# Performance work log

Hardware: AMD Instinct MI355X
Metric: run time of the kernel (lower is better)

Reference implementation:

```python
import jax, jax.numpy as jnp
import numpy as np

MASK_PROPORTION = 0.5
NEG_BIG = -99999999.0


def setup_inputs() -> dict:
    key = jax.random.key(0)
    k_x, k_w1, k_b1, k_w2, k_b2 = jax.random.split(key, 5)
    B, T, D, H = 32, 4096, 1024, 256
    x = jax.random.normal(k_x, (B, T, D), dtype=jnp.float32)
    s1 = 1.0 / np.sqrt(D)
    s2 = 1.0 / np.sqrt(H)
    W1 = jax.random.uniform(k_w1, (D, H), minval=-s1, maxval=s1, dtype=jnp.float32)
    b1 = jax.random.uniform(k_b1, (H,), minval=-s1, maxval=s1, dtype=jnp.float32)
    W2 = jax.random.uniform(k_w2, (H, 1), minval=-s2, maxval=s2, dtype=jnp.float32)
    b2 = jax.random.uniform(k_b2, (1,), minval=-s2, maxval=s2, dtype=jnp.float32)
    return {"x": x, "W1": W1, "b1": b1, "W2": W2, "b2": b2}


def reference(x, W1, b1, W2, b2):
    # e: [B, T, 1] attention scores from small MLP
    h = jnp.tanh(jnp.einsum("btd,dh->bth", x, W1) + b1)
    e = jnp.einsum("bth,ho->bto", h, W2) + b2  # [B, T, 1]

    T = e.shape[1]
    threshold_index = int(T * MASK_PROPORTION)
    sorted_e = jnp.sort(e, axis=1)
    threshold_value = sorted_e[:, threshold_index]          # [B, 1]
    # mask: +1 where e < threshold (kept), NEG_BIG where e >= threshold
    mask = jnp.where(e >= threshold_value[:, None, :], NEG_BIG, 1.0)
    e = e + mask
    beta = jax.nn.softmax(e, axis=1)                        # [B, T, 1]
    # bmm(beta^T, x) -> [B, 1, D], permute -> [B, D, 1], unsqueeze -> [B, D, 1, 1]
    out = jnp.einsum("bto,btd->bd", beta, x)
    return out[:, :, None, None]
```

## Files before the change

### kernel.cpp

```cpp
#include <hip/hip_runtime.h>
#include <hip/hip_bf16.h>
#include <math.h>

#define B_   32
#define T_   4096
#define D_   1024
#define H_   256
#define KTH  2048
#define SC   64
#define BM   128
#define BKE  32
#define NTE  (D_/BKE)
#define ABUF (BM*BKE)
#define BBUF (H_*BKE)
#define EPSB 4.0e-3f
#define MAXBAND 256
#define RB   4

typedef __attribute__((ext_vector_type(8))) short short8;
typedef __attribute__((ext_vector_type(4))) float f32x4;

#define FENCE4() asm volatile("s_waitcnt vmcnt(4) lgkmcnt(0)" ::: "memory")
#define FENCE0() asm volatile("s_waitcnt vmcnt(0) lgkmcnt(0)" ::: "memory")
#define BARRIER() __builtin_amdgcn_s_barrier()
#define SCHED()  __builtin_amdgcn_sched_barrier(0)
#define GLL(src, dst) __builtin_amdgcn_global_load_lds( \
    (const __attribute__((address_space(1))) unsigned int*)(src), \
    (__attribute__((address_space(3))) unsigned int*)(dst), 16, 0, 0)

__device__ inline unsigned f2s(float f) {
    unsigned u = __float_as_uint(f);
    return (u & 0x80000000u) ? ~u : (u | 0x80000000u);
}
__device__ inline float s2f(unsigned s) {
    unsigned x = (s & 0x80000000u) ? (s & 0x7fffffffu) : ~s;
    return __uint_as_float(x);
}
__device__ inline unsigned f2bf_rne(float f) {
    unsigned u = __float_as_uint(f);
    return (u + 0x7FFFu + ((u >> 16) & 1u)) >> 16;
}
__device__ inline unsigned pk2(float a, float b) {
    return f2bf_rne(a) | (f2bf_rne(b) << 16);
}
__device__ inline int block_sum_i(int v, int* sb, int tid) {
    #pragma unroll
    for (int o = 32; o; o >>= 1) v += __shfl_down(v, o);
    __syncthreads();
    if ((tid & 63) == 0) sb[tid >> 6] = v;
    __syncthreads();
    return sb[0] + sb[1] + sb[2] + sb[3];
}
__device__ inline float block_max_f(float v, float* sb, int tid) {
    #pragma unroll
    for (int o = 32; o; o >>= 1) v = fmaxf(v, __shfl_down(v, o));
    __syncthreads();
    if ((tid & 63) == 0) sb[tid >> 6] = v;
    __syncthreads();
    return fmaxf(fmaxf(sb[0], sb[1]), fmaxf(sb[2], sb[3]));
}
__device__ inline float block_sum_f(float v, float* sb, int tid) {
    #pragma unroll
    for (int o = 32; o; o >>= 1) v += __shfl_down(v, o);
    __syncthreads();
    if ((tid & 63) == 0) sb[tid >> 6] = v;
    __syncthreads();
    return sb[0] + sb[1] + sb[2] + sb[3];
}

__global__ __launch_bounds__(256) void k_w1t(const float* __restrict__ W1,
                                             ushort* __restrict__ Whi) {
    __shared__ float tile[32][33];
    const int kb = blockIdx.x * 32, nb = blockIdx.y * 32;
    const int tx = threadIdx.x & 31, ty = threadIdx.x >> 5;
    #pragma unroll
    for (int i = 0; i < 4; i++)
        tile[ty + 8*i][tx] = W1[(long)(kb + ty + 8*i) * H_ + nb + tx];
    __syncthreads();
    #pragma unroll
    for (int i = 0; i < 4; i++) {
        long o = (long)(nb + ty + 8*i) * D_ + kb + tx;
        Whi[o] = (ushort)f2bf_rne(tile[tx][ty + 8*i]);
    }
}

__global__ __launch_bounds__(512, 4) void k_e_mfma(
    const float* __restrict__ x,
    const ushort* __restrict__ Whi,
    const float* __restrict__ b1, const float* __restrict__ W2,
    const float* __restrict__ b2, float* __restrict__ e_out)
{
    __shared__ ushort sA[2][ABUF];
    __shared__ ushort sB[3][BBUF];
    __shared__ float  sRed[4][BM];

    const int tid  = threadIdx.x;
    const int lane = tid & 63;
    const int wv   = tid >> 6;
    const int wm   = wv >> 2, wn = wv & 3;
    const int l15  = lane & 15, lg = lane >> 4;
    const long row0 = (long)blockIdx.x * BM;

    const int ar = tid >> 2, aj = tid & 3;
    const float* aga = x + (row0 + ar) * (long)D_ + aj * 8;
    const int awo = (ar >> 4) * 512 + aj * 128 + (ar & 15) * 8;

    const int c0 = tid, c1 = tid + 512;
    const int bn0 = (c0 >> 6) * 16 + (c0 & 15), bk0 = (c0 >> 4) & 3;
    const int bn1 = (c1 >> 6) * 16 + (c1 & 15), bk1 = (c1 >> 4) & 3;
    const ushort* bga0 = Whi + (long)bn0 * D_ + bk0 * 8;
    const ushort* bga1 = Whi + (long)bn1 * D_ + bk1 * 8;
    const int bdst0 = c0 * 8, bdst1 = c1 * 8;

    int aoff[4], boff[4];
    #pragma unroll
    for (int fm = 0; fm < 4; fm++)
        aoff[fm] = (wm * 4 + fm) * 512 + lg * 128 + l15 * 8;
    #pragma unroll
    for (int fn = 0; fn < 4; fn++)
        boff[fn] = (wn * 4 + fn) * 512 + lg * 128 + l15 * 8;

    f32x4 acc[4][4];
    #pragma unroll
    for (int i = 0; i < 4; i++)
        #pragma unroll
        for (int j = 0; j < 4; j++) acc[i][j] = (f32x4){0.f, 0.f, 0.f, 0.f};

    ushort* sBb = (ushort*)sB;
    auto stageB = [&](int ko, int bi) {
        GLL(bga0 + ko, sBb + bi * BBUF + bdst0);
        GLL(bga1 + ko, sBb + bi * BBUF + bdst1);
    };
    auto writeA = [&](ushort* dst, const float4& a0, const float4& a1) {
        uint4 ap = make_uint4(pk2(a0.x, a0.y), pk2(a0.z, a0.w),
                              pk2(a1.x, a1.y), pk2(a1.z, a1.w));
        *(uint4*)&dst[awo] = ap;
    };
    auto compute = [&](const ushort* sa, const ushort* sb) {
        short8 bfr[4];
        #pragma unroll
        for (int fn = 0; fn < 4; fn++)
            bfr[fn] = *(const short8*)&sb[boff[fn]];
        __builtin_amdgcn_s_setprio(1);
        #pragma unroll
        for (int fm = 0; fm < 4; fm++) {
            short8 afr = *(const short8*)&sa[aoff[fm]];
            #pragma unroll
            for (int fn = 0; fn < 4; fn++)
                acc[fm][fn] = __builtin_amdgcn_mfma_f32_16x16x32_bf16(afr, bfr[fn], acc[fm][fn], 0, 0, 0);
        }
        __builtin_amdgcn_s_setprio(0);
    };

    float4 rA0a = *(const float4*)(aga);
    float4 rA0b = *(const float4*)(aga + 4);
    stageB(0, 0);
    float4 rA1a = *(const float4*)(aga + BKE);
    float4 rA1b = *(const float4*)(aga + BKE + 4);
    stageB(BKE, 1);
    writeA(sA[0], rA0a, rA0b);

    #pragma unroll 3
    for (int t = 0; t < NTE - 2; t += 2) {
        FENCE4(); BARRIER(); SCHED();
        {
            const int ko = (t + 2) * BKE;
            rA0a = *(const float4*)(aga + ko);
            rA0b = *(const float4*)(aga + ko + 4);
            stageB(ko, (t + 2) % 3);
            compute(sA[0], sBb + (t % 3) * BBUF);
            writeA(sA[1], rA1a, rA1b);
        }
        FENCE4(); BARRIER(); SCHED();
        {
            const int ko = (t + 3) * BKE;
            rA1a = *(const float4*)(aga + ko);
            rA1b = *(const float4*)(aga + ko + 4);
            stageB(ko, (t + 3) % 3);
            compute(sA[1], sBb + ((t + 1) % 3) * BBUF);
            writeA(sA[0], rA0a, rA0b);
        }
    }
    FENCE4(); BARRIER(); SCHED();
    compute(sA[0], sBb + ((NTE - 2) % 3) * BBUF);
    writeA(sA[1], rA1a, rA1b);
    FENCE0(); BARRIER(); SCHED();
    compute(sA[1], sBb + ((NTE - 1) % 3) * BBUF);

    float b1v[4], w2v[4];
    #pragma unroll
    for (int fn = 0; fn < 4; fn++) {
        int j = wn * 64 + fn * 16 + l15;
        b1v[fn] = b1[j]; w2v[fn] = W2[j];
    }
    #pragma unroll
    for (int fm = 0; fm < 4; fm++) {
        #pragma unroll
        for (int r = 0; r < 4; r++) {
            float s = 0.f;
            #pragma unroll
            for (int fn = 0; fn < 4; fn++)
                s += tanhf(acc[fm][fn][r] + b1v[fn]) * w2v[fn];
            s += __shfl_xor(s, 1); s += __shfl_xor(s, 2);
            s += __shfl_xor(s, 4); s += __shfl_xor(s, 8);
            if (l15 == 0) sRed[wn][wm * 64 + fm * 16 + lg * 4 + r] = s;
        }
    }
    __syncthreads();
    if (tid < BM)
        e_out[row0 + tid] = sRed[0][tid] + sRed[1][tid] + sRed[2][tid] + sRed[3][tid] + b2[0];
}

template<int BUILD>
__global__ __launch_bounds__(256) void k_thresh(const float* __restrict__ e,
                                                int* __restrict__ counts,
                                                int* __restrict__ list,
                                                int* __restrict__ sidx,
                                                float* __restrict__ sval,
                                                int* __restrict__ scount) {
    __shared__ int   sbi[4];
    __shared__ float sbf[4];
    __shared__ int   wsum[4];
    __shared__ int   scnt;
    const int b = blockIdx.x, tid = threadIdx.x;
    const int lane = tid & 63, wid = tid >> 6;
    const float* eb = e + (long)b * T_;
    const int t0 = tid * 16;

    float fe[16]; unsigned ue[16];
    #pragma unroll
    for (int i = 0; i < 16; i += 4) {
        float4 v = *(const float4*)(eb + t0 + i);
        fe[i] = v.x; fe[i+1] = v.y; fe[i+2] = v.z; fe[i+3] = v.w;
    }
    #pragma unroll
    for (int i = 0; i < 16; i++) ue[i] = f2s(fe[i]);

    unsigned lo = 0u, hi = 0xFFFFFFFFu;
    while (lo < hi) {
        unsigned mid = lo + ((hi - lo) >> 1);
        int c = 0;
        #pragma unroll
        for (int i = 0; i < 16; i++) c += (ue[i] <= mid) ? 1 : 0;
        int total = block_sum_i(c, sbi, tid);
        if (total >= KTH + 1) hi = mid; else lo = mid + 1;
    }
    const float thr = s2f(lo);

    if (BUILD) {
        if (tid == 0) scnt = 0;
        __syncthreads();
        #pragma unroll
        for (int i = 0; i < 16; i++) {
            if (fabsf(fe[i] - thr) <= EPSB) {
                int p = atomicAdd(&scnt, 1);
                if (p < MAXBAND) list[b * MAXBAND + p] = t0 + i;
            }
        }
        __syncthreads();
        if (tid == 0) counts[b] = scnt < MAXBAND ? scnt : MAXBAND;
    } else {
        float m = -INFINITY;
        #pragma unroll
        for (int i = 0; i < 16; i++) if (fe[i] < thr) m = fmaxf(m, fe[i]);
        m = block_max_f(m, sbf, tid);
        float s = 0.f;
        #pragma unroll
        for (int i = 0; i < 16; i++) if (fe[i] < thr) s += expf(fe[i] - m);
        s = block_sum_f(s, sbf, tid);
        const float inv = 1.0f / s;

        int c = 0;
        #pragma unroll
        for (int i = 0; i < 16; i++) c += (fe[i] < thr) ? 1 : 0;
        int p = c;
        #pragma unroll
        for (int o = 1; o < 64; o <<= 1) {
            int y = __shfl_up(p, o);
            if (lane >= o) p += y;
        }
        if (lane == 63) wsum[wid] = p;
        __syncthreads();
        int base = 0;
        #pragma unroll
        for (int w = 0; w < 4; w++) base += (w < wid) ? wsum[w] : 0;
        int pos = base + p - c;
        #pragma unroll
        for (int i = 0; i < 16; i++) {
            if (fe[i] < thr) {
                sidx[(long)b * T_ + pos] = t0 + i;
                sval[(long)b * T_ + pos] = expf(fe[i] - m) * inv;
                pos++;
            }
        }
        if (tid == 0) scount[b] = wsum[0] + wsum[1] + wsum[2] + wsum[3];
    }
}

__global__ __launch_bounds__(256) void k_refine(const float* __restrict__ x,
        const float* __restrict__ W1, const float* __restrict__ b1,
        const float* __restrict__ W2, const float* __restrict__ b2,
        const int* __restrict__ counts, const int* __restrict__ list,
        float* __restrict__ e) {
    const int b   = blockIdx.y;
    const int blk = blockIdx.x;
    const int cnt = counts[b];
    const int tid = threadIdx.x;
    __shared__ float xs[RB][D_];
    __shared__ float sbf[4];

    for (int g = blk * RB; g < cnt; g += 16 * RB) {
        const int nr = min(RB, cnt - g);
        for (int j = 0; j < nr; j++) {
            const int t = list[b * MAXBAND + g + j];
            *(float4*)&xs[j][tid * 4] =
                *(const float4*)&x[((long)b * T_ + t) * D_ + tid * 4];
        }
        __syncthreads();

        float a0 = 0.f, a1 = 0.f, a2 = 0.f, a3 = 0.f;
        for (int k0 = 0; k0 < D_; k0 += 4) {
            const float w0 = W1[(long)(k0 + 0) * H_ + tid];
            const float w1v = W1[(long)(k0 + 1) * H_ + tid];
            const float w2q = W1[(long)(k0 + 2) * H_ + tid];
            const float w3 = W1[(long)(k0 + 3) * H_ + tid];
            {
                float4 xv = *(const float4*)&xs[0][k0];
                a0 = fmaf(xv.x, w0, a0); a0 = fmaf(xv.y, w1v, a0);
                a0 = fmaf(xv.z, w2q, a0); a0 = fmaf(xv.w, w3, a0);
            }
            {
                float4 xv = *(const float4*)&xs[1][k0];
                a1 = fmaf(xv.x, w0, a1); a1 = fmaf(xv.y, w1v, a1);
                a1 = fmaf(xv.z, w2q, a1); a1 = fmaf(xv.w, w3, a1);
            }
            {
                float4 xv = *(const float4*)&xs[2][k0];
                a2 = fmaf(xv.x, w0, a2); a2 = fmaf(xv.y, w1v, a2);
                a2 = fmaf(xv.z, w2q, a2); a2 = fmaf(xv.w, w3, a2);
            }
            {
                float4 xv = *(const float4*)&xs[3][k0];
                a3 = fmaf(xv.x, w0, a3); a3 = fmaf(xv.y, w1v, a3);
                a3 = fmaf(xv.z, w2q, a3); a3 = fmaf(xv.w, w3, a3);
            }
        }

        float aj[RB] = {a0, a1, a2, a3};
        for (int j = 0; j < nr; j++) {
            float v = tanhf(aj[j] + b1[tid]) * W2[tid];
            float tot = block_sum_f(v, sbf, tid);
            if (tid == 0) {
                const int t = list[b * MAXBAND + g + j];
                e[(long)b * T_ + t] = tot + b2[0];
            }
            __syncthreads();
        }
        __syncthreads();
    }
}

__global__ __launch_bounds__(256) void k_pv(const float* __restrict__ x,
                                            const int* __restrict__ sidx,
                                            const float* __restrict__ sval,
                                            const int* __restrict__ scount,
                                            float* __restrict__ partial) {
    const int c = blockIdx.x, b = blockIdx.y, tid = threadIdx.x;
    const int cnt = scount[b];
    const int len = (cnt + SC - 1) / SC;
    const int k0 = c * len;
    const int nl = min(len, cnt - k0);
    __shared__ int   si[32];
    __shared__ float sv[32];
    if (tid < nl) {
        si[tid] = sidx[(long)b * T_ + k0 + tid];
        sv[tid] = sval[(long)b * T_ + k0 + tid];
    }
    __syncthreads();

    float4 acc = {0.f, 0.f, 0.f, 0.f};
    const float* xb = x + (long)b * T_ * D_ + tid * 4;
    #pragma unroll 4
    for (int k = 0; k < nl; k++) {
        const float w = sv[k];
        float4 v = *(const float4*)(xb + (long)si[k] * D_);
        acc.x = fmaf(w, v.x, acc.x);
        acc.y = fmaf(w, v.y, acc.y);
        acc.z = fmaf(w, v.z, acc.z);
        acc.w = fmaf(w, v.w, acc.w);
    }
    *(float4*)&partial[(((long)b * SC) + c) * D_ + tid * 4] = acc;
}

__global__ __launch_bounds__(256) void k_red(const float* __restrict__ partial,
                                             float* __restrict__ out) {
    const int b = blockIdx.x, tid = threadIdx.x;
    float4 acc = {0.f, 0.f, 0.f, 0.f};
    #pragma unroll
    for (int c = 0; c < SC; c++) {
        float4 v = *(const float4*)&partial[(((long)b * SC) + c) * D_ + tid * 4];
        acc.x += v.x; acc.y += v.y; acc.z += v.z; acc.w += v.w;
    }
    *(float4*)&out[(long)b * D_ + tid * 4] = acc;
}

extern "C" void kernel_launch(void* const* d_in, const int* in_sizes, int n_in,
                              void* d_out, int out_size, void* d_ws, size_t ws_size,
                              hipStream_t stream) {
    const float* x  = (const float*)d_in[0];
    const float* W1 = (const float*)d_in[1];
    const float* b1 = (const float*)d_in[2];
    const float* W2 = (const float*)d_in[3];
    const float* b2 = (const float*)d_in[4];
    float* out = (float*)d_out;

    char* ws = (char*)d_ws;
    float* e       = (float*)ws;  ws += (size_t)B_ * T_ * 4;
    int*   sidx    = (int*)ws;    ws += (size_t)B_ * T_ * 4;
    float* sval    = (float*)ws;  ws += (size_t)B_ * T_ * 4;
    float* partial = (float*)ws;  ws += (size_t)B_ * SC * D_ * 4;
    ushort* Whi    = (ushort*)ws; ws += (size_t)H_ * D_ * 2;
    int* counts    = (int*)ws;    ws += 128;
    int* scountp   = (int*)ws;    ws += 128;
    int* list      = (int*)ws;

    k_w1t<<<dim3(D_ / 32, H_ / 32), 256, 0, stream>>>(W1, Whi);
    k_e_mfma<<<(B_ * T_) / BM, 512, 0, stream>>>(x, Whi, b1, W2, b2, e);
    k_thresh<1><<<B_, 256, 0, stream>>>(e, counts, list, sidx, sval, scountp);
    k_refine<<<dim3(16, B_), 256, 0, stream>>>(x, W1, b1, W2, b2, counts, list, e);
    k_thresh<0><<<B_, 256, 0, stream>>>(e, counts, list, sidx, sval, scountp);
    k_pv<<<dim3(SC, B_), 256, 0, stream>>>(x, sidx, sval, scountp, partial);
    k_red<<<B_, 256, 0, stream>>>(partial, out);
}
```

Before: 322.0 us.

## Pre-convert x to bf16 and stream A tiles via direct LDS loads

Adds a pre-pass that converts the whole input x to bf16 in workspace. The MFMA scoring kernel then loads A tiles with global_load_lds through a uniform 3-stage ring instead of converting fp32 registers in-loop, and the weighted-sum kernel reads bf16 rows. This removes in-loop conversion and halves the bytes those two kernels read, but adds a full extra read and write pass over x and lowers the precision of the output accumulation.

After: 416.2 us. 29.2% more time.

```diff
diff --git a/kernel.cpp b/kernel.cpp
--- a/kernel.cpp
+++ b/kernel.cpp
@@ -11,8 +11,8 @@
 #define BM   128
 #define BKE  32
 #define NTE  (D_/BKE)
-#define ABUF (BM*BKE)
-#define BBUF (H_*BKE)
+#define ASZ  (BM*BKE)
+#define BSZ  (H_*BKE)
 #define EPSB 4.0e-3f
 #define MAXBAND 256
 #define RB   4
@@ -20,10 +20,9 @@
 typedef __attribute__((ext_vector_type(8))) short short8;
 typedef __attribute__((ext_vector_type(4))) float f32x4;
 
-#define FENCE4() asm volatile("s_waitcnt vmcnt(4) lgkmcnt(0)" ::: "memory")
+#define FENCE3() asm volatile("s_waitcnt vmcnt(3) lgkmcnt(0)" ::: "memory")
 #define FENCE0() asm volatile("s_waitcnt vmcnt(0) lgkmcnt(0)" ::: "memory")
 #define BARRIER() __builtin_amdgcn_s_barrier()
-#define SCHED()  __builtin_amdgcn_sched_barrier(0)
 #define GLL(src, dst) __builtin_amdgcn_global_load_lds( \
     (const __attribute__((address_space(1))) unsigned int*)(src), \
     (__attribute__((address_space(3))) unsigned int*)(dst), 16, 0, 0)
@@ -43,6 +42,9 @@
 __device__ inline unsigned pk2(float a, float b) {
     return f2bf_rne(a) | (f2bf_rne(b) << 16);
 }
+__device__ inline float bf2f(ushort u) {
+    return __uint_as_float(((unsigned)u) << 16);
+}
 __device__ inline int block_sum_i(int v, int* sb, int tid) {
     #pragma unroll
     for (int o = 32; o; o >>= 1) v += __shfl_down(v, o);
@@ -66,6 +68,19 @@
     if ((tid & 63) == 0) sb[tid >> 6] = v;
     __syncthreads();
     return sb[0] + sb[1] + sb[2] + sb[3];
+}
+
+__global__ __launch_bounds__(256) void k_cvt(const float* __restrict__ x,
+                                             ushort* __restrict__ xb) {
+    const long n = (long)B_ * T_ * D_;
+    const long stride = (long)gridDim.x * 256 * 8;
+    for (long i = ((long)blockIdx.x * 256 + threadIdx.x) * 8; i < n; i += stride) {
+        float4 a = *(const float4*)(x + i);
+        float4 b = *(const float4*)(x + i + 4);
+        uint4 p = make_uint4(pk2(a.x, a.y), pk2(a.z, a.w),
+                             pk2(b.x, b.y), pk2(b.z, b.w));
+        *(uint4*)(xb + i) = p;
+    }
 }
 
 __global__ __launch_bounds__(256) void k_w1t(const float* __restrict__ W1,
@@ -85,13 +100,13 @@
 }
 
 __global__ __launch_bounds__(512, 4) void k_e_mfma(
-    const float* __restrict__ x,
+    const ushort* __restrict__ xb,
     const ushort* __restrict__ Whi,
     const float* __restrict__ b1, const float* __restrict__ W2,
     const float* __restrict__ b2, float* __restrict__ e_out)
 {
-    __shared__ ushort sA[2][ABUF];
-    __shared__ ushort sB[3][BBUF];
+    __shared__ ushort sA[3 * ASZ];
+    __shared__ ushort sB[3 * BSZ];
     __shared__ float  sRed[4][BM];
 
     const int tid  = threadIdx.x;
@@ -101,16 +116,17 @@
     const int l15  = lane & 15, lg = lane >> 4;
     const long row0 = (long)blockIdx.x * BM;
 
-    const int ar = tid >> 2, aj = tid & 3;
-    const float* aga = x + (row0 + ar) * (long)D_ + aj * 8;
-    const int awo = (ar >> 4) * 512 + aj * 128 + (ar & 15) * 8;
-
-    const int c0 = tid, c1 = tid + 512;
-    const int bn0 = (c0 >> 6) * 16 + (c0 & 15), bk0 = (c0 >> 4) & 3;
-    const int bn1 = (c1 >> 6) * 16 + (c1 & 15), bk1 = (c1 >> 4) & 3;
-    const ushort* bga0 = Whi + (long)bn0 * D_ + bk0 * 8;
-    const ushort* bga1 = Whi + (long)bn1 * D_ + bk1 * 8;
-    const int bdst0 = c0 * 8, bdst1 = c1 * 8;
+    const int arow = (tid >> 6) * 16 + (tid & 15);
+    const int akc  = (tid >> 4) & 3;
+    const ushort* asrc = xb + (row0 + arow) * (long)D_ + akc * 8;
+    const int adst = tid * 8;
+
+    const int c1 = tid + 512;
+    const int bn0 = (tid >> 6) * 16 + (tid & 15), bk0 = (tid >> 4) & 3;
+    const int bn1 = (c1 >> 6) * 16 + (c1 & 15),  bk1 = (c1 >> 4) & 3;
+    const ushort* bsrc0 = Whi + (long)bn0 * D_ + bk0 * 8;
+    const ushort* bsrc1 = Whi + (long)bn1 * D_ + bk1 * 8;
+    const int bdst0 = tid * 8, bdst1 = c1 * 8;
 
     int aoff[4], boff[4];
     #pragma unroll
@@ -126,17 +142,15 @@
         #pragma unroll
         for (int j = 0; j < 4; j++) acc[i][j] = (f32x4){0.f, 0.f, 0.f, 0.f};
 
-    ushort* sBb = (ushort*)sB;
-    auto stageB = [&](int ko, int bi) {
-        GLL(bga0 + ko, sBb + bi * BBUF + bdst0);
-        GLL(bga1 + ko, sBb + bi * BBUF + bdst1);
+    auto stage = [&](int t, int bi) {
+        const int ko = t * BKE;
+        GLL(asrc + ko,  sA + bi * ASZ + adst);
+        GLL(bsrc0 + ko, sB + bi * BSZ + bdst0);
+        GLL(bsrc1 + ko, sB + bi * BSZ + bdst1);
     };
-    auto writeA = [&](ushort* dst, const float4& a0, const float4& a1) {
-        uint4 ap = make_uint4(pk2(a0.x, a0.y), pk2(a0.z, a0.w),
-                              pk2(a1.x, a1.y), pk2(a1.z, a1.w));
-        *(uint4*)&dst[awo] = ap;
-    };
-    auto compute = [&](const ushort* sa, const ushort* sb) {
+    auto compute = [&](int bi) {
+        const ushort* sa = sA + bi * ASZ;
+        const ushort* sb = sB + bi * BSZ;
         short8 bfr[4];
         #pragma unroll
         for (int fn = 0; fn < 4; fn++)
@@ -152,40 +166,22 @@
         __builtin_amdgcn_s_setprio(0);
     };
 
-    float4 rA0a = *(const float4*)(aga);
-    float4 rA0b = *(const float4*)(aga + 4);
-    stageB(0, 0);
-    float4 rA1a = *(const float4*)(aga + BKE);
-    float4 rA1b = *(const float4*)(aga + BKE + 4);
-    stageB(BKE, 1);
-    writeA(sA[0], rA0a, rA0b);
-
-    #pragma unroll 3
-    for (int t = 0; t < NTE - 2; t += 2) {
-        FENCE4(); BARRIER(); SCHED();
-        {
-            const int ko = (t + 2) * BKE;
-            rA0a = *(const float4*)(aga + ko);
-            rA0b = *(const float4*)(aga + ko + 4);
-            stageB(ko, (t + 2) % 3);
-            compute(sA[0], sBb + (t % 3) * BBUF);
-            writeA(sA[1], rA1a, rA1b);
-        }
-        FENCE4(); BARRIER(); SCHED();
-        {
-            const int ko = (t + 3) * BKE;
-            rA1a = *(const float4*)(aga + ko);
-            rA1b = *(const float4*)(aga + ko + 4);
-            stageB(ko, (t + 3) % 3);
-            compute(sA[1], sBb + ((t + 1) % 3) * BBUF);
-            writeA(sA[0], rA0a, rA0b);
-        }
-    }
-    FENCE4(); BARRIER(); SCHED();
-    compute(sA[0], sBb + ((NTE - 2) % 3) * BBUF);
-    writeA(sA[1], rA1a, rA1b);
-    FENCE0(); BARRIER(); SCHED();
-    compute(sA[1], sBb + ((NTE - 1) % 3) * BBUF);
+    stage(0, 0);
+    stage(1, 1);
+
+    int bi = 0;
+    for (int t = 0; t <= NTE - 3; ++t) {
+        FENCE3(); BARRIER();
+        const int nb = (bi + 2 >= 3) ? bi - 1 : bi + 2;
+        stage(t + 2, nb);
+        compute(bi);
+        bi = (bi + 1 == 3) ? 0 : bi + 1;
+    }
+    FENCE3(); BARRIER();
+    compute(bi);
+    bi = (bi + 1 == 3) ? 0 : bi + 1;
+    FENCE0(); BARRIER();
+    compute(bi);
 
     float b1v[4], w2v[4];
     #pragma unroll
@@ -360,7 +356,7 @@
     }
 }
 
-__global__ __launch_bounds__(256) void k_pv(const float* __restrict__ x,
+__global__ __launch_bounds__(256) void k_pv(const ushort* __restrict__ xb,
                                             const int* __restrict__ sidx,
                                             const float* __restrict__ sval,
                                             const int* __restrict__ scount,
@@ -379,15 +375,15 @@
     __syncthreads();
 
     float4 acc = {0.f, 0.f, 0.f, 0.f};
-    const float* xb = x + (long)b * T_ * D_ + tid * 4;
+    const ushort* xbb = xb + (long)b * T_ * D_ + tid * 4;
     #pragma unroll 4
     for (int k = 0; k < nl; k++) {
         const float w = sv[k];
-        float4 v = *(const float4*)(xb + (long)si[k] * D_);
-        acc.x = fmaf(w, v.x, acc.x);
-        acc.y = fmaf(w, v.y, acc.y);
-        acc.z = fmaf(w, v.z, acc.z);
-        acc.w = fmaf(w, v.w, acc.w);
+        ushort4 v = *(const ushort4*)(xbb + (long)si[k] * D_);
+        acc.x = fmaf(w, bf2f(v.x), acc.x);
+        acc.y = fmaf(w, bf2f(v.y), acc.y);
+        acc.z = fmaf(w, bf2f(v.z), acc.z);
+        acc.w = fmaf(w, bf2f(v.w), acc.w);
     }
     *(float4*)&partial[(((long)b * SC) + c) * D_ + tid * 4] = acc;
 }
@@ -422,13 +418,15 @@
     ushort* Whi    = (ushort*)ws; ws += (size_t)H_ * D_ * 2;
     int* counts    = (int*)ws;    ws += 128;
     int* scountp   = (int*)ws;    ws += 128;
-    int* list      = (int*)ws;
-
+    int* list      = (int*)ws;    ws += (size_t)B_ * MAXBAND * 4;
+    ushort* xb16   = (ushort*)(((uintptr_t)ws + 255) & ~(uintptr_t)255);
+
+    k_cvt<<<2048, 256, 0, stream>>>(x, xb16);
     k_w1t<<<dim3(D_ / 32, H_ / 32), 256, 0, stream>>>(W1, Whi);
-    k_e_mfma<<<(B_ * T_) / BM, 512, 0, stream>>>(x, Whi, b1, W2, b2, e);
+    k_e_mfma<<<(B_ * T_) / BM, 512, 0, stream>>>(xb16, Whi, b1, W2, b2, e);
     k_thresh<1><<<B_, 256, 0, stream>>>(e, counts, list, sidx, sval, scountp);
     k_refine<<<dim3(16, B_), 256, 0, stream>>>(x, W1, b1, W2, b2, counts, list, e);
     k_thresh<0><<<B_, 256, 0, stream>>>(e, counts, list, sidx, sval, scountp);
-    k_pv<<<dim3(SC, B_), 256, 0, stream>>>(x, sidx, sval, scountp, partial);
+    k_pv<<<dim3(SC, B_), 256, 0, stream>>>(xb16, sidx, sval, scountp, partial);
     k_red<<<B_, 256, 0, stream>>>(partial, out);
 }
```

## Restructure e-GEMM mainloop with BK=64 double buffering and split-phase LDS reads

Applied to the files above, without the earlier changes.

Rewrites the x·W1 MFMA main loop to use K-tiles of 64 instead of 32, with two LDS buffers for A and B instead of a 2/3-buffer scheme. Each tile is processed in two half-K phases. Fragments are preloaded into registers before the barriers, and B is staged and A global loads issued for later tiles in between. The launch-bounds occupancy hint is dropped. The aim is fewer barriers per K element and better overlap of global loads with MFMA, at the cost of more LDS per block, more registers, and a barrier schedule that is more fragile.

Result: slower. 392.1 us (+21.8%).

```diff
diff --git a/kernel.cpp b/kernel.cpp
--- a/kernel.cpp
+++ b/kernel.cpp
@@ -9,10 +9,8 @@
 #define KTH  2048
 #define SC   64
 #define BM   128
-#define BKE  32
-#define NTE  (D_/BKE)
-#define ABUF (BM*BKE)
-#define BBUF (H_*BKE)
+#define BKL  64
+#define NKT  (D_/BKL)
 #define EPSB 4.0e-3f
 #define MAXBAND 256
 #define RB   4
@@ -20,10 +18,10 @@
 typedef __attribute__((ext_vector_type(8))) short short8;
 typedef __attribute__((ext_vector_type(4))) float f32x4;
 
-#define FENCE4() asm volatile("s_waitcnt vmcnt(4) lgkmcnt(0)" ::: "memory")
+#define FENCEA() asm volatile("s_waitcnt vmcnt(4) lgkmcnt(0)" ::: "memory")
 #define FENCE0() asm volatile("s_waitcnt vmcnt(0) lgkmcnt(0)" ::: "memory")
+#define LGKM0()  asm volatile("s_waitcnt lgkmcnt(0)" ::: "memory")
 #define BARRIER() __builtin_amdgcn_s_barrier()
-#define SCHED()  __builtin_amdgcn_sched_barrier(0)
 #define GLL(src, dst) __builtin_amdgcn_global_load_lds( \
     (const __attribute__((address_space(1))) unsigned int*)(src), \
     (__attribute__((address_space(3))) unsigned int*)(dst), 16, 0, 0)
@@ -42,6 +40,9 @@
 }
 __device__ inline unsigned pk2(float a, float b) {
     return f2bf_rne(a) | (f2bf_rne(b) << 16);
+}
+__device__ inline float bf2f(ushort u) {
+    return __uint_as_float(((unsigned)u) << 16);
 }
 __device__ inline int block_sum_i(int v, int* sb, int tid) {
     #pragma unroll
@@ -84,14 +85,14 @@
     }
 }
 
-__global__ __launch_bounds__(512, 4) void k_e_mfma(
+__global__ __launch_bounds__(512) void k_e_mfma(
     const float* __restrict__ x,
     const ushort* __restrict__ Whi,
     const float* __restrict__ b1, const float* __restrict__ W2,
     const float* __restrict__ b2, float* __restrict__ e_out)
 {
-    __shared__ ushort sA[2][ABUF];
-    __shared__ ushort sB[3][BBUF];
+    __shared__ ushort sA[2][BM * BKL];
+    __shared__ ushort sB[2][H_ * BKL];
     __shared__ float  sRed[4][BM];
 
     const int tid  = threadIdx.x;
@@ -101,24 +102,30 @@
     const int l15  = lane & 15, lg = lane >> 4;
     const long row0 = (long)blockIdx.x * BM;
 
-    const int ar = tid >> 2, aj = tid & 3;
-    const float* aga = x + (row0 + ar) * (long)D_ + aj * 8;
-    const int awo = (ar >> 4) * 512 + aj * 128 + (ar & 15) * 8;
-
-    const int c0 = tid, c1 = tid + 512;
-    const int bn0 = (c0 >> 6) * 16 + (c0 & 15), bk0 = (c0 >> 4) & 3;
-    const int bn1 = (c1 >> 6) * 16 + (c1 & 15), bk1 = (c1 >> 4) & 3;
-    const ushort* bga0 = Whi + (long)bn0 * D_ + bk0 * 8;
-    const ushort* bga1 = Whi + (long)bn1 * D_ + bk1 * 8;
-    const int bdst0 = c0 * 8, bdst1 = c1 * 8;
-
-    int aoff[4], boff[4];
-    #pragma unroll
-    for (int fm = 0; fm < 4; fm++)
-        aoff[fm] = (wm * 4 + fm) * 512 + lg * 128 + l15 * 8;
-    #pragma unroll
-    for (int fn = 0; fn < 4; fn++)
-        boff[fn] = (wn * 4 + fn) * 512 + lg * 128 + l15 * 8;
+    const int ar = tid >> 2, aq = tid & 3;
+    const float* aga = x + (row0 + ar) * (long)D_ + aq * 16;
+    const int awo0 = (ar >> 4) * 1024 + (aq * 2) * 128 + (ar & 15) * 8;
+    const int awo1 = awo0 + 128;
+
+    const ushort* bsrc[4];
+    #pragma unroll
+    for (int j = 0; j < 4; j++) {
+        const int L = wv * 4 + j;
+        const int n  = (L >> 1) * 16 + (lane & 15);
+        const int kc = (L & 1) * 4 + (lane >> 4);
+        bsrc[j] = Whi + (long)n * D_ + kc * 8;
+    }
+    const int bb = wv * 2048;
+
+    int aoff[2][4], boff[2][4];
+    #pragma unroll
+    for (int kk = 0; kk < 2; kk++) {
+        #pragma unroll
+        for (int f = 0; f < 4; f++) {
+            aoff[kk][f] = (wm * 4 + f) * 1024 + (kk * 4 + lg) * 128 + l15 * 8;
+            boff[kk][f] = (wn * 4 + f) * 1024 + (kk * 4 + lg) * 128 + l15 * 8;
+        }
+    }
 
     f32x4 acc[4][4];
     #pragma unroll
@@ -126,66 +133,84 @@
         #pragma unroll
         for (int j = 0; j < 4; j++) acc[i][j] = (f32x4){0.f, 0.f, 0.f, 0.f};
 
-    ushort* sBb = (ushort*)sB;
-    auto stageB = [&](int ko, int bi) {
-        GLL(bga0 + ko, sBb + bi * BBUF + bdst0);
-        GLL(bga1 + ko, sBb + bi * BBUF + bdst1);
-    };
-    auto writeA = [&](ushort* dst, const float4& a0, const float4& a1) {
-        uint4 ap = make_uint4(pk2(a0.x, a0.y), pk2(a0.z, a0.w),
-                              pk2(a1.x, a1.y), pk2(a1.z, a1.w));
-        *(uint4*)&dst[awo] = ap;
-    };
-    auto compute = [&](const ushort* sa, const ushort* sb) {
-        short8 bfr[4];
-        #pragma unroll
-        for (int fn = 0; fn < 4; fn++)
-            bfr[fn] = *(const short8*)&sb[boff[fn]];
-        __builtin_amdgcn_s_setprio(1);
-        #pragma unroll
-        for (int fm = 0; fm < 4; fm++) {
-            short8 afr = *(const short8*)&sa[aoff[fm]];
-            #pragma unroll
-            for (int fn = 0; fn < 4; fn++)
-                acc[fm][fn] = __builtin_amdgcn_mfma_f32_16x16x32_bf16(afr, bfr[fn], acc[fm][fn], 0, 0, 0);
-        }
-        __builtin_amdgcn_s_setprio(0);
-    };
-
-    float4 rA0a = *(const float4*)(aga);
-    float4 rA0b = *(const float4*)(aga + 4);
-    stageB(0, 0);
-    float4 rA1a = *(const float4*)(aga + BKE);
-    float4 rA1b = *(const float4*)(aga + BKE + 4);
-    stageB(BKE, 1);
-    writeA(sA[0], rA0a, rA0b);
-
-    #pragma unroll 3
-    for (int t = 0; t < NTE - 2; t += 2) {
-        FENCE4(); BARRIER(); SCHED();
-        {
-            const int ko = (t + 2) * BKE;
-            rA0a = *(const float4*)(aga + ko);
-            rA0b = *(const float4*)(aga + ko + 4);
-            stageB(ko, (t + 2) % 3);
-            compute(sA[0], sBb + (t % 3) * BBUF);
-            writeA(sA[1], rA1a, rA1b);
-        }
-        FENCE4(); BARRIER(); SCHED();
-        {
-            const int ko = (t + 3) * BKE;
-            rA1a = *(const float4*)(aga + ko);
-            rA1b = *(const float4*)(aga + ko + 4);
-            stageB(ko, (t + 3) % 3);
-            compute(sA[1], sBb + ((t + 1) % 3) * BBUF);
-            writeA(sA[0], rA0a, rA0b);
-        }
-    }
-    FENCE4(); BARRIER(); SCHED();
-    compute(sA[0], sBb + ((NTE - 2) % 3) * BBUF);
-    writeA(sA[1], rA1a, rA1b);
-    FENCE0(); BARRIER(); SCHED();
-    compute(sA[1], sBb + ((NTE - 1) % 3) * BBUF);
+    float4 Ra0, Ra1, Ra2, Ra3, Rb0, Rb1, Rb2, Rb3;
+
+#define STAGEB(T, BUF) do { \
+    _Pragma("unroll") \
+    for (int j = 0; j < 4; j++) GLL(bsrc[j] + (T) * BKL, &sB[BUF][bb + j * 512]); \
+} while (0)
+
+#define WRITEA(BUF, S0, S1, S2, S3) do { \
+    uint4 _u0 = make_uint4(pk2((S0).x,(S0).y), pk2((S0).z,(S0).w), \
+                           pk2((S1).x,(S1).y), pk2((S1).z,(S1).w)); \
+    uint4 _u1 = make_uint4(pk2((S2).x,(S2).y), pk2((S2).z,(S2).w), \
+                           pk2((S3).x,(S3).y), pk2((S3).z,(S3).w)); \
+    *(uint4*)&sA[BUF][awo0] = _u0; \
+    *(uint4*)&sA[BUF][awo1] = _u1; \
+} while (0)
+
+#define MFMA16(AF, BF) do { \
+    __builtin_amdgcn_s_setprio(1); \
+    _Pragma("unroll") \
+    for (int fm = 0; fm < 4; fm++) \
+        _Pragma("unroll") \
+        for (int fn = 0; fn < 4; fn++) \
+            acc[fm][fn] = __builtin_amdgcn_mfma_f32_16x16x32_bf16((AF)[fm], (BF)[fn], acc[fm][fn], 0, 0, 0); \
+    __builtin_amdgcn_s_setprio(0); \
+} while (0)
+
+#define TILE_BODY(T, C, L0, L1, L2, L3, W0, W1v, W2v, W3) do { \
+    const int _tn = ((T) + 1 < NKT) ? (T) + 1 : NKT - 1; \
+    const int _tp = ((T) + 2 < NKT) ? (T) + 2 : NKT - 1; \
+     \
+    short8 _a0[4], _b0[4]; \
+    _Pragma("unroll") \
+    for (int f = 0; f < 4; f++) _b0[f] = *(const short8*)&sB[C][boff[0][f]]; \
+    _Pragma("unroll") \
+    for (int f = 0; f < 4; f++) _a0[f] = *(const short8*)&sA[C][aoff[0][f]]; \
+    STAGEB(_tn, (C) ^ 1); \
+    L0 = *(const float4*)(aga + _tp * BKL); \
+    L1 = *(const float4*)(aga + _tp * BKL + 4); \
+    BARRIER(); LGKM0(); \
+    MFMA16(_a0, _b0); \
+    BARRIER(); \
+     \
+    short8 _a1[4], _b1[4]; \
+    _Pragma("unroll") \
+    for (int f = 0; f < 4; f++) _b1[f] = *(const short8*)&sB[C][boff[1][f]]; \
+    _Pragma("unroll") \
+    for (int f = 0; f < 4; f++) _a1[f] = *(const short8*)&sA[C][aoff[1][f]]; \
+    L2 = *(const float4*)(aga + _tp * BKL + 8); \
+    L3 = *(const float4*)(aga + _tp * BKL + 12); \
+    WRITEA((C) ^ 1, W0, W1v, W2v, W3); \
+    FENCEA(); BARRIER(); \
+    MFMA16(_a1, _b1); \
+    BARRIER(); \
+} while (0)
+
+    Ra0 = *(const float4*)(aga + 0);
+    Ra1 = *(const float4*)(aga + 4);
+    Ra2 = *(const float4*)(aga + 8);
+    Ra3 = *(const float4*)(aga + 12);
+    STAGEB(0, 0);
+    STAGEB(1, 1);
+    Rb0 = *(const float4*)(aga + BKL + 0);
+    Rb1 = *(const float4*)(aga + BKL + 4);
+    Rb2 = *(const float4*)(aga + BKL + 8);
+    Rb3 = *(const float4*)(aga + BKL + 12);
+    WRITEA(0, Ra0, Ra1, Ra2, Ra3);
+    FENCE0(); BARRIER();
+
+    for (int t = 0; t < NKT; t += 2) {
+        TILE_BODY(t,     0, Ra0, Ra1, Ra2, Ra3, Rb0, Rb1, Rb2, Rb3);
+        TILE_BODY(t + 1, 1, Rb0, Rb1, Rb2, Rb3, Ra0, Ra1, Ra2, Ra3);
+    }
+    FENCE0(); BARRIER();
+
+#undef TILE_BODY
+#undef MFMA16
+#undef WRITEA
+#undef STAGEB
 
     float b1v[4], w2v[4];
     #pragma unroll
```

## Restructure score GEMM into 64-row barrier-free tiles with register-resident A

Applied to the files above, without the earlier changes.

The x·W1 MFMA kernel drops from 128-row tiles with 512 threads to 64-row tiles with 256 threads. Each wave now loads the x rows straight into registers and converts them to bf16 in-register, instead of staging them through LDS. Each wave double-buffers only its own slice of W1 in LDS through global_load_lds, so the block-wide barriers go away and a single vmcnt wait handles synchronisation. The aim is to cut LDS traffic and barrier stalls. In exchange, all four waves re-read the same x rows from global memory (relying on cache hits), and each W1 tile is reused across fewer rows.

New measurement: 526.6 us. 1.64x slower.

```diff
diff --git a/kernel.cpp b/kernel.cpp
--- a/kernel.cpp
+++ b/kernel.cpp
@@ -8,11 +8,9 @@
 #define H_   256
 #define KTH  2048
 #define SC   64
-#define BM   128
-#define BKE  32
-#define NTE  (D_/BKE)
-#define ABUF (BM*BKE)
-#define BBUF (H_*BKE)
+#define BK   32
+#define NT   (D_/BK)
+#define BSZ  (H_*BK)
 #define EPSB 4.0e-3f
 #define MAXBAND 256
 #define RB   4
@@ -20,10 +18,7 @@
 typedef __attribute__((ext_vector_type(8))) short short8;
 typedef __attribute__((ext_vector_type(4))) float f32x4;
 
-#define FENCE4() asm volatile("s_waitcnt vmcnt(4) lgkmcnt(0)" ::: "memory")
-#define FENCE0() asm volatile("s_waitcnt vmcnt(0) lgkmcnt(0)" ::: "memory")
-#define BARRIER() __builtin_amdgcn_s_barrier()
-#define SCHED()  __builtin_amdgcn_sched_barrier(0)
+#define VM8()  asm volatile("s_waitcnt vmcnt(8)" ::: "memory")
 #define GLL(src, dst) __builtin_amdgcn_global_load_lds( \
     (const __attribute__((address_space(1))) unsigned int*)(src), \
     (__attribute__((address_space(3))) unsigned int*)(dst), 16, 0, 0)
@@ -84,38 +79,39 @@
     }
 }
 
-__global__ __launch_bounds__(512, 4) void k_e_mfma(
+__global__ __launch_bounds__(256, 3) void k_e_mfma(
     const float* __restrict__ x,
     const ushort* __restrict__ Whi,
     const float* __restrict__ b1, const float* __restrict__ W2,
     const float* __restrict__ b2, float* __restrict__ e_out)
 {
-    __shared__ ushort sA[2][ABUF];
-    __shared__ ushort sB[3][BBUF];
-    __shared__ float  sRed[4][BM];
+    __shared__ ushort sB[2 * BSZ];
+    __shared__ float  sRed[4][64];
 
     const int tid  = threadIdx.x;
     const int lane = tid & 63;
-    const int wv   = tid >> 6;
-    const int wm   = wv >> 2, wn = wv & 3;
+    const int wn   = tid >> 6;
     const int l15  = lane & 15, lg = lane >> 4;
-    const long row0 = (long)blockIdx.x * BM;
-
-    const int ar = tid >> 2, aj = tid & 3;
-    const float* aga = x + (row0 + ar) * (long)D_ + aj * 8;
-    const int awo = (ar >> 4) * 512 + aj * 128 + (ar & 15) * 8;
-
-    const int c0 = tid, c1 = tid + 512;
-    const int bn0 = (c0 >> 6) * 16 + (c0 & 15), bk0 = (c0 >> 4) & 3;
-    const int bn1 = (c1 >> 6) * 16 + (c1 & 15), bk1 = (c1 >> 4) & 3;
-    const ushort* bga0 = Whi + (long)bn0 * D_ + bk0 * 8;
-    const ushort* bga1 = Whi + (long)bn1 * D_ + bk1 * 8;
-    const int bdst0 = c0 * 8, bdst1 = c1 * 8;
-
-    int aoff[4], boff[4];
+    const long row0 = (long)blockIdx.x * 64;
+
+    const float* aptr[4];
     #pragma unroll
     for (int fm = 0; fm < 4; fm++)
-        aoff[fm] = (wm * 4 + fm) * 512 + lg * 128 + l15 * 8;
+        aptr[fm] = x + (row0 + fm * 16 + l15) * (long)D_ + lg * 8;
+
+    const ushort* bsrc[4];
+    int bdst[4];
+    #pragma unroll
+    for (int j = 0; j < 4; j++) {
+        const int L0 = (wn * 4 + j) * 64;
+        const int L  = L0 + lane;
+        const int n  = (L >> 6) * 16 + (L & 15);
+        const int kc = (L >> 4) & 3;
+        bsrc[j] = Whi + (long)n * D_ + kc * 8;
+        bdst[j] = L0 * 8;
+    }
+
+    int boff[4];
     #pragma unroll
     for (int fn = 0; fn < 4; fn++)
         boff[fn] = (wn * 4 + fn) * 512 + lg * 128 + l15 * 8;
@@ -126,66 +122,55 @@
         #pragma unroll
         for (int j = 0; j < 4; j++) acc[i][j] = (f32x4){0.f, 0.f, 0.f, 0.f};
 
-    ushort* sBb = (ushort*)sB;
-    auto stageB = [&](int ko, int bi) {
-        GLL(bga0 + ko, sBb + bi * BBUF + bdst0);
-        GLL(bga1 + ko, sBb + bi * BBUF + bdst1);
-    };
-    auto writeA = [&](ushort* dst, const float4& a0, const float4& a1) {
-        uint4 ap = make_uint4(pk2(a0.x, a0.y), pk2(a0.z, a0.w),
-                              pk2(a1.x, a1.y), pk2(a1.z, a1.w));
-        *(uint4*)&dst[awo] = ap;
-    };
-    auto compute = [&](const ushort* sa, const ushort* sb) {
+    float4 ArA[4], ArB[4];
+
+    #pragma unroll
+    for (int j = 0; j < 4; j++) GLL(bsrc[j], &sB[bdst[j]]);
+    #pragma unroll
+    for (int fm = 0; fm < 4; fm++) {
+        ArA[fm] = *(const float4*)(aptr[fm]);
+        ArB[fm] = *(const float4*)(aptr[fm] + 4);
+    }
+
+    for (int t = 0; t < NT; ++t) {
+        const ushort* sbp = sB + (t & 1) * BSZ;
+        ushort* sbn = sB + ((t & 1) ^ 1) * BSZ;
+        VM8();
         short8 bfr[4];
         #pragma unroll
         for (int fn = 0; fn < 4; fn++)
-            bfr[fn] = *(const short8*)&sb[boff[fn]];
-        __builtin_amdgcn_s_setprio(1);
-        #pragma unroll
-        for (int fm = 0; fm < 4; fm++) {
-            short8 afr = *(const short8*)&sa[aoff[fm]];
+            bfr[fn] = *(const short8*)&sbp[boff[fn]];
+        if (t + 1 < NT) {
+            const int ko = (t + 1) * BK;
             #pragma unroll
-            for (int fn = 0; fn < 4; fn++)
-                acc[fm][fn] = __builtin_amdgcn_mfma_f32_16x16x32_bf16(afr, bfr[fn], acc[fm][fn], 0, 0, 0);
-        }
-        __builtin_amdgcn_s_setprio(0);
-    };
-
-    float4 rA0a = *(const float4*)(aga);
-    float4 rA0b = *(const float4*)(aga + 4);
-    stageB(0, 0);
-    float4 rA1a = *(const float4*)(aga + BKE);
-    float4 rA1b = *(const float4*)(aga + BKE + 4);
-    stageB(BKE, 1);
-    writeA(sA[0], rA0a, rA0b);
-
-    #pragma unroll 3
-    for (int t = 0; t < NTE - 2; t += 2) {
-        FENCE4(); BARRIER(); SCHED();
-        {
-            const int ko = (t + 2) * BKE;
-            rA0a = *(const float4*)(aga + ko);
-            rA0b = *(const float4*)(aga + ko + 4);
-            stageB(ko, (t + 2) % 3);
-            compute(sA[0], sBb + (t % 3) * BBUF);
-            writeA(sA[1], rA1a, rA1b);
-        }
-        FENCE4(); BARRIER(); SCHED();
-        {
-            const int ko = (t + 3) * BKE;
-            rA1a = *(const float4*)(aga + ko);
-            rA1b = *(const float4*)(aga + ko + 4);
-            stageB(ko, (t + 3) % 3);
-            compute(sA[1], sBb + ((t + 1) % 3) * BBUF);
-            writeA(sA[0], rA0a, rA0b);
-        }
-    }
-    FENCE4(); BARRIER(); SCHED();
-    compute(sA[0], sBb + ((NTE - 2) % 3) * BBUF);
-    writeA(sA[1], rA1a, rA1b);
-    FENCE0(); BARRIER(); SCHED();
-    compute(sA[1], sBb + ((NTE - 1) % 3) * BBUF);
+            for (int j = 0; j < 4; j++) GLL(bsrc[j] + ko, &sbn[bdst[j]]);
+            #pragma unroll
+            for (int fm = 0; fm < 4; fm++) {
+                union { uint4 u4; short8 s8; } cv;
+                cv.u4 = make_uint4(pk2(ArA[fm].x, ArA[fm].y), pk2(ArA[fm].z, ArA[fm].w),
+                                   pk2(ArB[fm].x, ArB[fm].y), pk2(ArB[fm].z, ArB[fm].w));
+                ArA[fm] = *(const float4*)(aptr[fm] + ko);
+                ArB[fm] = *(const float4*)(aptr[fm] + ko + 4);
+                __builtin_amdgcn_s_setprio(1);
+                #pragma unroll
+                for (int fn = 0; fn < 4; fn++)
+                    acc[fm][fn] = __builtin_amdgcn_mfma_f32_16x16x32_bf16(cv.s8, bfr[fn], acc[fm][fn], 0, 0, 0);
+                __builtin_amdgcn_s_setprio(0);
+            }
+        } else {
+            #pragma unroll
+            for (int fm = 0; fm < 4; fm++) {
+                union { uint4 u4; short8 s8; } cv;
+                cv.u4 = make_uint4(pk2(ArA[fm].x, ArA[fm].y), pk2(ArA[fm].z, ArA[fm].w),
+                                   pk2(ArB[fm].x, ArB[fm].y), pk2(ArB[fm].z, ArB[fm].w));
+                __builtin_amdgcn_s_setprio(1);
+                #pragma unroll
+                for (int fn = 0; fn < 4; fn++)
+                    acc[fm][fn] = __builtin_amdgcn_mfma_f32_16x16x32_bf16(cv.s8, bfr[fn], acc[fm][fn], 0, 0, 0);
+                __builtin_amdgcn_s_setprio(0);
+            }
+        }
+    }
 
     float b1v[4], w2v[4];
     #pragma unroll
@@ -203,11 +188,11 @@
                 s += tanhf(acc[fm][fn][r] + b1v[fn]) * w2v[fn];
             s += __shfl_xor(s, 1); s += __shfl_xor(s, 2);
             s += __shfl_xor(s, 4); s += __shfl_xor(s, 8);
-            if (l15 == 0) sRed[wn][wm * 64 + fm * 16 + lg * 4 + r] = s;
-        }
-    }
-    __syncthreads();
-    if (tid < BM)
+            if (l15 == 0) sRed[wn][fm * 16 + lg * 4 + r] = s;
+        }
+    }
+    __syncthreads();
+    if (tid < 64)
         e_out[row0 + tid] = sRed[0][tid] + sRed[1][tid] + sRed[2][tid] + sRed[3][tid] + b2[0];
 }
 
@@ -425,7 +410,7 @@
     int* list      = (int*)ws;
 
     k_w1t<<<dim3(D_ / 32, H_ / 32), 256, 0, stream>>>(W1, Whi);
-    k_e_mfma<<<(B_ * T_) / BM, 512, 0, stream>>>(x, Whi, b1, W2, b2, e);
+    k_e_mfma<<<(B_ * T_) / 64, 256, 0, stream>>>(x, Whi, b1, W2, b2, e);
     k_thresh<1><<<B_, 256, 0, stream>>>(e, counts, list, sidx, sval, scountp);
     k_refine<<<dim3(16, B_), 256, 0, stream>>>(x, W1, b1, W2, b2, counts, list, e);
     k_thresh<0><<<B_, 256, 0, stream>>>(e, counts, list, sidx, sval, scountp);
```
